# Optimization experiments

Hardware: AMD Instinct MI355X
Metric: run time of the kernel (lower is better)

## Reference

```python
import jax, jax.numpy as jnp
import numpy as np

N = 8192      # nodes
E = 262144    # edges (avg degree 32)
IN_DIM = 512
H1 = 256
H2 = 128


def _graph_conv(x, src, dst, W, b, act):
    """DGL GraphConv with norm='both', allow_zero_in_degree=True.
    h = D_in^{-1/2} * A @ (D_out^{-1/2} * x @ W) + b, then activation.
    Degrees clamped to min 1 (DGL behavior)."""
    ones = jnp.ones((src.shape[0],), dtype=x.dtype)
    deg_out = jax.ops.segment_sum(ones, src, num_segments=N)
    deg_in = jax.ops.segment_sum(ones, dst, num_segments=N)
    norm_src = jnp.maximum(deg_out, 1.0) ** -0.5  # [N]
    norm_dst = jnp.maximum(deg_in, 1.0) ** -0.5   # [N]
    # apply weight before aggregation (out_feats < in_feats, as DGL does)
    h = (x * norm_src[:, None]) @ W               # [N, out]
    agg = jax.ops.segment_sum(h[src], dst, num_segments=N)  # gather-scatter SpMM
    return act(agg * norm_dst[:, None] + b)


def setup_inputs() -> dict:
    key = jax.random.key(0)
    ks = jax.random.split(key, 7)
    features = jax.random.normal(ks[0], (N, IN_DIM), dtype=jnp.float32)
    src = jax.random.randint(ks[1], (E,), 0, N)
    dst = jax.random.randint(ks[2], (E,), 0, N)
    W1 = jax.random.normal(ks[3], (IN_DIM, H1), dtype=jnp.float32) * (1.0 / np.sqrt(IN_DIM))
    b1 = jnp.zeros((H1,), dtype=jnp.float32)
    W2 = jax.random.normal(ks[4], (H1, H2), dtype=jnp.float32) * (1.0 / np.sqrt(H1))
    b2 = jnp.zeros((H2,), dtype=jnp.float32)
    return {"features": features, "src": src, "dst": dst,
            "W1": W1, "b1": b1, "W2": W2, "b2": b2}


def reference(features, src, dst, W1, b1, W2, b2):
    x = _graph_conv(features, src, dst, W1, b1, jax.nn.relu)
    emb = _graph_conv(x, src, dst, W2, b2, lambda a: a)
    logits = jax.nn.sigmoid(emb @ emb.T)  # [N, N] dense reconstruction
    return (emb, logits)
```

## Files before the change

kernel.cpp:

```cpp
#include <hip/hip_runtime.h>

#define NN 8192
#define EE 262144
#define IN_DIM 512
#define HD1 256
#define HD2 128

typedef __attribute__((ext_vector_type(8))) short bf16x8;
typedef __attribute__((ext_vector_type(4))) float f32x4;

__device__ inline unsigned short f2bf(float f) {
    unsigned int u = __builtin_bit_cast(unsigned int, f);
    u += 0x7fffu + ((u >> 16) & 1u);
    return (unsigned short)(u >> 16);
}


__global__ void deg_kernel(const int* __restrict__ src, const int* __restrict__ dst,
                           int* __restrict__ deg_out, int* __restrict__ deg_in) {
    int e = blockIdx.x * blockDim.x + threadIdx.x;
    if (e < EE) {
        atomicAdd(&deg_out[src[e]], 1);
        atomicAdd(&deg_in[dst[e]], 1);
    }
}

__global__ void norm_kernel(const int* __restrict__ deg_out, const int* __restrict__ deg_in,
                            float* __restrict__ norm_src, float* __restrict__ norm_dst) {
    int i = blockIdx.x * blockDim.x + threadIdx.x;
    if (i < NN) {
        int dout = deg_out[i]; if (dout < 1) dout = 1;
        int din  = deg_in[i];  if (din  < 1) din  = 1;
        norm_src[i] = rsqrtf((float)dout);
        norm_dst[i] = rsqrtf((float)din);
    }
}

__global__ void scan_kernel(const int* __restrict__ counts, int* __restrict__ row_start) {
    __shared__ int sums[256];
    int t = threadIdx.x;
    int base = t * 32;
    int local[32];
    int s = 0;
    for (int i = 0; i < 32; i++) { local[i] = s; s += counts[base + i]; }
    sums[t] = s;
    __syncthreads();
    for (int off = 1; off < 256; off <<= 1) {
        int v = (t >= off) ? sums[t - off] : 0;
        __syncthreads();
        sums[t] += v;
        __syncthreads();
    }
    int coff = (t == 0) ? 0 : sums[t - 1];
    for (int i = 0; i < 32; i++) row_start[base + i] = coff + local[i];
    if (t == 255) row_start[NN] = sums[255];
}

__global__ void fill_kernel(const int* __restrict__ src, const int* __restrict__ dst,
                            const int* __restrict__ row_start, int* __restrict__ cursor,
                            int* __restrict__ eidx) {
    int e = blockIdx.x * blockDim.x + threadIdx.x;
    if (e < EE) {
        int d = dst[e];
        int pos = atomicAdd(&cursor[d], 1);
        eidx[row_start[d] + pos] = src[e];
    }
}


__global__ void scale_cast_kernel(const float4* __restrict__ x, const float* __restrict__ norm_src,
                                  ushort4* __restrict__ out) {
    int idx = blockIdx.x * blockDim.x + threadIdx.x;
    if (idx < NN * IN_DIM / 4) {
        float ns = norm_src[idx >> 7];
        float4 v = x[idx];
        ushort4 o;
        o.x = f2bf(v.x * ns); o.y = f2bf(v.y * ns);
        o.z = f2bf(v.z * ns); o.w = f2bf(v.w * ns);
        out[idx] = o;
    }
}

__global__ void transpose_cast_kernel(const float* __restrict__ W, unsigned short* __restrict__ Wt,
                                      int K, int Nc) {
    int idx = blockIdx.x * blockDim.x + threadIdx.x;
    if (idx < K * Nc) {
        int n = idx / K;
        int k = idx - n * K;
        Wt[idx] = f2bf(W[k * Nc + n]);
    }
}

template <int EPI>
__global__ __launch_bounds__(256) void gemm_tn(const short* __restrict__ A,
                                               const short* __restrict__ B,
                                               float* __restrict__ C, int N, int K) {
    int wave = threadIdx.x >> 6;
    int lane = threadIdx.x & 63;
    int wr = wave >> 1, wc = wave & 1;
    int row0 = blockIdx.y * 128 + wr * 64;
    int col0 = blockIdx.x * 128 + wc * 64;
    int l15 = lane & 15, q = lane >> 4;

    f32x4 acc[4][4] = {};
    const short* Abase = A + (size_t)(row0 + l15) * K + q * 8;
    const short* Bbase = B + (size_t)(col0 + l15) * K + q * 8;
    int nk = K >> 5;
    for (int ks = 0; ks < nk; ks++) {
        bf16x8 a[4], b[4];
#pragma unroll
        for (int t = 0; t < 4; t++) {
            a[t] = *(const bf16x8*)(Abase + (size_t)t * 16 * K + ks * 32);
            b[t] = *(const bf16x8*)(Bbase + (size_t)t * 16 * K + ks * 32);
        }
#pragma unroll
        for (int ti = 0; ti < 4; ti++)
#pragma unroll
            for (int tj = 0; tj < 4; tj++)
                acc[ti][tj] = __builtin_amdgcn_mfma_f32_16x16x32_bf16(a[ti], b[tj], acc[ti][tj], 0, 0, 0);
    }
#pragma unroll
    for (int ti = 0; ti < 4; ti++) {
#pragma unroll
        for (int tj = 0; tj < 4; tj++) {
#pragma unroll
            for (int r = 0; r < 4; r++) {
                int row = row0 + ti * 16 + q * 4 + r;
                int col = col0 + tj * 16 + l15;
                float v = acc[ti][tj][r];
                if (EPI == 1) v = __builtin_amdgcn_rcpf(1.0f + __expf(-v));
                C[(size_t)row * N + col] = v;
            }
        }
    }
}


__global__ void spmm1_kernel(const float* __restrict__ h1, const int* __restrict__ row_start,
                             const int* __restrict__ eidx, const float* __restrict__ norm_dst,
                             const float* __restrict__ norm_src, const float* __restrict__ b1,
                             unsigned short* __restrict__ x1n) {
    int r = blockIdx.x;
    int t = threadIdx.x;
    int s = row_start[r], e = row_start[r + 1];
    float sum = 0.0f;
    int i = s;
    for (; i + 4 <= e; i += 4) {
        int n0 = eidx[i], n1 = eidx[i + 1], n2 = eidx[i + 2], n3 = eidx[i + 3];
        float v0 = h1[n0 * HD1 + t];
        float v1 = h1[n1 * HD1 + t];
        float v2 = h1[n2 * HD1 + t];
        float v3 = h1[n3 * HD1 + t];
        sum += v0 + v1 + v2 + v3;
    }
    for (; i < e; i++) sum += h1[eidx[i] * HD1 + t];
    float x = sum * norm_dst[r] + b1[t];
    x = fmaxf(x, 0.0f) * norm_src[r];
    x1n[r * HD1 + t] = f2bf(x);
}

__global__ void spmm2_kernel(const float* __restrict__ h2, const int* __restrict__ row_start,
                             const int* __restrict__ eidx, const float* __restrict__ norm_dst,
                             const float* __restrict__ b2, float* __restrict__ emb,
                             unsigned short* __restrict__ embb) {
    int r = blockIdx.x;
    int t = threadIdx.x;
    int s = row_start[r], e = row_start[r + 1];
    float sum = 0.0f;
    int i = s;
    for (; i + 4 <= e; i += 4) {
        int n0 = eidx[i], n1 = eidx[i + 1], n2 = eidx[i + 2], n3 = eidx[i + 3];
        float v0 = h2[n0 * HD2 + t];
        float v1 = h2[n1 * HD2 + t];
        float v2 = h2[n2 * HD2 + t];
        float v3 = h2[n3 * HD2 + t];
        sum += v0 + v1 + v2 + v3;
    }
    for (; i < e; i++) sum += h2[eidx[i] * HD2 + t];
    float x = sum * norm_dst[r] + b2[t];
    emb[r * HD2 + t] = x;
    embb[r * HD2 + t] = f2bf(x);
}


extern "C" void kernel_launch(void* const* d_in, const int* in_sizes, int n_in,
                              void* d_out, int out_size, void* d_ws, size_t ws_size,
                              hipStream_t stream) {
    const float* features = (const float*)d_in[0];
    const int* src = (const int*)d_in[1];
    const int* dst = (const int*)d_in[2];
    const float* W1 = (const float*)d_in[3];
    const float* b1 = (const float*)d_in[4];
    const float* W2 = (const float*)d_in[5];
    const float* b2 = (const float*)d_in[6];

    char* ws = (char*)d_ws;
    size_t o = 0;
    auto alloc = [&](size_t bytes) -> char* {
        char* p = ws + o;
        o = (o + bytes + 255) & ~(size_t)255;
        return p;
    };
    int* deg_out = (int*)alloc(NN * 4);
    int* deg_in  = (int*)alloc(NN * 4);
    int* cursor  = (int*)alloc(NN * 4);
    float* norm_src = (float*)alloc(NN * 4);
    float* norm_dst = (float*)alloc(NN * 4);
    int* row_start  = (int*)alloc((NN + 1) * 4);
    int* eidx       = (int*)alloc(EE * 4);
    unsigned short* xn  = (unsigned short*)alloc((size_t)NN * IN_DIM * 2);
    unsigned short* w1t = (unsigned short*)alloc((size_t)HD1 * IN_DIM * 2);
    unsigned short* w2t = (unsigned short*)alloc((size_t)HD2 * HD1 * 2);
    float* h1 = (float*)alloc((size_t)NN * HD1 * 4);
    unsigned short* x1n = (unsigned short*)alloc((size_t)NN * HD1 * 2);
    float* h2 = (float*)alloc((size_t)NN * HD2 * 4);
    unsigned short* embb = (unsigned short*)alloc((size_t)NN * HD2 * 2);

    float* emb_out = (float*)d_out;
    float* logits_out = emb_out + (size_t)NN * HD2;

    hipMemsetAsync(deg_out, 0, (size_t)NN * 4 * 3, stream);

    deg_kernel<<<EE / 256, 256, 0, stream>>>(src, dst, deg_out, deg_in);
    norm_kernel<<<NN / 256, 256, 0, stream>>>(deg_out, deg_in, norm_src, norm_dst);
    scan_kernel<<<1, 256, 0, stream>>>(deg_in, row_start);
    fill_kernel<<<EE / 256, 256, 0, stream>>>(src, dst, row_start, cursor, eidx);

    scale_cast_kernel<<<(NN * IN_DIM / 4) / 256, 256, 0, stream>>>(
        (const float4*)features, norm_src, (ushort4*)xn);
    transpose_cast_kernel<<<(IN_DIM * HD1 + 255) / 256, 256, 0, stream>>>(W1, w1t, IN_DIM, HD1);
    transpose_cast_kernel<<<(HD1 * HD2 + 255) / 256, 256, 0, stream>>>(W2, w2t, HD1, HD2);

    gemm_tn<0><<<dim3(HD1 / 128, NN / 128), 256, 0, stream>>>(
        (const short*)xn, (const short*)w1t, h1, HD1, IN_DIM);
    spmm1_kernel<<<NN, HD1, 0, stream>>>(h1, row_start, eidx, norm_dst, norm_src, b1, x1n);

    gemm_tn<0><<<dim3(HD2 / 128, NN / 128), 256, 0, stream>>>(
        (const short*)x1n, (const short*)w2t, h2, HD2, HD1);
    spmm2_kernel<<<NN, HD2, 0, stream>>>(h2, row_start, eidx, norm_dst, b2, emb_out, embb);

    gemm_tn<1><<<dim3(NN / 128, NN / 128), 256, 0, stream>>>(
        (const short*)embb, (const short*)embb, logits_out, NN, HD2);
}
```

Before: 433.3 us.

## Vectorize logits stores, use bf16 intermediates, and fuse preprocessing kernels

The logits GEMM epilogue now writes float4 rows by exploiting the symmetry of emb·embᵀ, so each lane stores a transposed contiguous 4-float chunk instead of scattered scalars. The h1 and h2 intermediates are stored as bf16, with the source-norm scaling folded into the first GEMM epilogue. The SpMM kernels switch to one wave per row with vectorized bf16 gathers. The norm and scan kernels are merged, and the casts are merged into one kernel. This reduces store transactions and gather bandwidth, at the cost of extra bf16 rounding of intermediates and reliance on output symmetry.

After: 448.4 us. 1.03x slower.

```diff
diff --git a/kernel.cpp b/kernel.cpp
--- a/kernel.cpp
+++ b/kernel.cpp
@@ -13,6 +13,9 @@
     unsigned int u = __builtin_bit_cast(unsigned int, f);
     u += 0x7fffu + ((u >> 16) & 1u);
     return (unsigned short)(u >> 16);
+}
+__device__ inline float bf2f(unsigned short u) {
+    return __builtin_bit_cast(float, ((unsigned int)u) << 16);
 }
 
 
@@ -25,24 +28,20 @@
     }
 }
 
-__global__ void norm_kernel(const int* __restrict__ deg_out, const int* __restrict__ deg_in,
-                            float* __restrict__ norm_src, float* __restrict__ norm_dst) {
-    int i = blockIdx.x * blockDim.x + threadIdx.x;
-    if (i < NN) {
-        int dout = deg_out[i]; if (dout < 1) dout = 1;
-        int din  = deg_in[i];  if (din  < 1) din  = 1;
-        norm_src[i] = rsqrtf((float)dout);
-        norm_dst[i] = rsqrtf((float)din);
-    }
-}
-
-__global__ void scan_kernel(const int* __restrict__ counts, int* __restrict__ row_start) {
+__global__ void scan_norm_kernel(const int* __restrict__ deg_in, const int* __restrict__ deg_out,
+                                 int* __restrict__ row_start,
+                                 float* __restrict__ norm_src, float* __restrict__ norm_dst) {
     __shared__ int sums[256];
     int t = threadIdx.x;
     int base = t * 32;
+    int4 c[8];
+#pragma unroll
+    for (int i = 0; i < 8; i++) c[i] = ((const int4*)deg_in)[t * 8 + i];
+    const int* ci = (const int*)c;
     int local[32];
     int s = 0;
-    for (int i = 0; i < 32; i++) { local[i] = s; s += counts[base + i]; }
+#pragma unroll
+    for (int i = 0; i < 32; i++) { local[i] = s; s += ci[i]; }
     sums[t] = s;
     __syncthreads();
     for (int off = 1; off < 256; off <<= 1) {
@@ -52,8 +51,16 @@
         __syncthreads();
     }
     int coff = (t == 0) ? 0 : sums[t - 1];
+#pragma unroll
     for (int i = 0; i < 32; i++) row_start[base + i] = coff + local[i];
     if (t == 255) row_start[NN] = sums[255];
+    for (int i = 0; i < 32; i++) {
+        int idx = i * 256 + t;
+        int dout = deg_out[idx]; if (dout < 1) dout = 1;
+        int din  = deg_in[idx];  if (din  < 1) din  = 1;
+        norm_src[idx] = rsqrtf((float)dout);
+        norm_dst[idx] = rsqrtf((float)din);
+    }
 }
 
 __global__ void fill_kernel(const int* __restrict__ src, const int* __restrict__ dst,
@@ -68,33 +75,38 @@
 }
 
 
-__global__ void scale_cast_kernel(const float4* __restrict__ x, const float* __restrict__ norm_src,
-                                  ushort4* __restrict__ out) {
-    int idx = blockIdx.x * blockDim.x + threadIdx.x;
-    if (idx < NN * IN_DIM / 4) {
-        float ns = norm_src[idx >> 7];
+#define XN_QUADS (NN * IN_DIM / 4)
+#define W1_ELEMS (IN_DIM * HD1)
+#define W2_ELEMS (HD1 * HD2)
+
+__global__ void cast_all_kernel(const float4* __restrict__ x, ushort4* __restrict__ xn,
+                                const float* __restrict__ W1, unsigned short* __restrict__ w1t,
+                                const float* __restrict__ W2, unsigned short* __restrict__ w2t) {
+    int idx = blockIdx.x * 256 + threadIdx.x;
+    if (idx < XN_QUADS) {
         float4 v = x[idx];
         ushort4 o;
-        o.x = f2bf(v.x * ns); o.y = f2bf(v.y * ns);
-        o.z = f2bf(v.z * ns); o.w = f2bf(v.w * ns);
-        out[idx] = o;
-    }
-}
-
-__global__ void transpose_cast_kernel(const float* __restrict__ W, unsigned short* __restrict__ Wt,
-                                      int K, int Nc) {
-    int idx = blockIdx.x * blockDim.x + threadIdx.x;
-    if (idx < K * Nc) {
-        int n = idx / K;
-        int k = idx - n * K;
-        Wt[idx] = f2bf(W[k * Nc + n]);
+        o.x = f2bf(v.x); o.y = f2bf(v.y); o.z = f2bf(v.z); o.w = f2bf(v.w);
+        xn[idx] = o;
+    } else if (idx < XN_QUADS + W1_ELEMS) {
+        int j = idx - XN_QUADS;
+        int n = j >> 9;
+        int k = j & (IN_DIM - 1);
+        w1t[j] = f2bf(W1[k * HD1 + n]);
+    } else if (idx < XN_QUADS + W1_ELEMS + W2_ELEMS) {
+        int j = idx - XN_QUADS - W1_ELEMS;
+        int n = j >> 8;
+        int k = j & (HD1 - 1);
+        w2t[j] = f2bf(W2[k * HD2 + n]);
     }
 }
 
 template <int EPI>
 __global__ __launch_bounds__(256) void gemm_tn(const short* __restrict__ A,
                                                const short* __restrict__ B,
-                                               float* __restrict__ C, int N, int K) {
+                                               void* __restrict__ Cv,
+                                               const float* __restrict__ rownorm,
+                                               int N, int K) {
     int wave = threadIdx.x >> 6;
     int lane = threadIdx.x & 63;
     int wr = wave >> 1, wc = wave & 1;
@@ -119,67 +131,105 @@
             for (int tj = 0; tj < 4; tj++)
                 acc[ti][tj] = __builtin_amdgcn_mfma_f32_16x16x32_bf16(a[ti], b[tj], acc[ti][tj], 0, 0, 0);
     }
-#pragma unroll
-    for (int ti = 0; ti < 4; ti++) {
-#pragma unroll
-        for (int tj = 0; tj < 4; tj++) {
-#pragma unroll
-            for (int r = 0; r < 4; r++) {
-                int row = row0 + ti * 16 + q * 4 + r;
-                int col = col0 + tj * 16 + l15;
-                float v = acc[ti][tj][r];
-                if (EPI == 1) v = __builtin_amdgcn_rcpf(1.0f + __expf(-v));
-                C[(size_t)row * N + col] = v;
+
+    if (EPI == 1) {
+        float* C = (float*)Cv;
+#pragma unroll
+        for (int ti = 0; ti < 4; ti++) {
+#pragma unroll
+            for (int tj = 0; tj < 4; tj++) {
+                int row = col0 + tj * 16 + l15;
+                int colb = row0 + ti * 16 + q * 4;
+                float4 v;
+                float* vp = (float*)&v;
+#pragma unroll
+                for (int r = 0; r < 4; r++) {
+                    float x = acc[ti][tj][r];
+                    vp[r] = __builtin_amdgcn_rcpf(1.0f + __expf(-x));
+                }
+                *(float4*)(C + (size_t)row * N + colb) = v;
             }
         }
-    }
-}
-
-
-__global__ void spmm1_kernel(const float* __restrict__ h1, const int* __restrict__ row_start,
+    } else {
+        unsigned short* C = (unsigned short*)Cv;
+#pragma unroll
+        for (int ti = 0; ti < 4; ti++) {
+#pragma unroll
+            for (int tj = 0; tj < 4; tj++) {
+#pragma unroll
+                for (int r = 0; r < 4; r++) {
+                    int row = row0 + ti * 16 + q * 4 + r;
+                    int col = col0 + tj * 16 + l15;
+                    float v = acc[ti][tj][r];
+                    if (EPI == 2) v *= rownorm[row];
+                    C[(size_t)row * N + col] = f2bf(v);
+                }
+            }
+        }
+    }
+}
+
+
+__global__ void spmm1_kernel(const ushort4* __restrict__ h1b, const int* __restrict__ row_start,
                              const int* __restrict__ eidx, const float* __restrict__ norm_dst,
-                             const float* __restrict__ norm_src, const float* __restrict__ b1,
-                             unsigned short* __restrict__ x1n) {
-    int r = blockIdx.x;
-    int t = threadIdx.x;
+                             const float* __restrict__ norm_src, const float4* __restrict__ b1,
+                             ushort4* __restrict__ x1n) {
+    int lane = threadIdx.x & 63;
+    int r = blockIdx.x * 4 + (threadIdx.x >> 6);
     int s = row_start[r], e = row_start[r + 1];
-    float sum = 0.0f;
+    float sx = 0.f, sy = 0.f, sz = 0.f, sw = 0.f;
     int i = s;
-    for (; i + 4 <= e; i += 4) {
-        int n0 = eidx[i], n1 = eidx[i + 1], n2 = eidx[i + 2], n3 = eidx[i + 3];
-        float v0 = h1[n0 * HD1 + t];
-        float v1 = h1[n1 * HD1 + t];
-        float v2 = h1[n2 * HD1 + t];
-        float v3 = h1[n3 * HD1 + t];
-        sum += v0 + v1 + v2 + v3;
-    }
-    for (; i < e; i++) sum += h1[eidx[i] * HD1 + t];
-    float x = sum * norm_dst[r] + b1[t];
-    x = fmaxf(x, 0.0f) * norm_src[r];
-    x1n[r * HD1 + t] = f2bf(x);
-}
-
-__global__ void spmm2_kernel(const float* __restrict__ h2, const int* __restrict__ row_start,
+    for (; i + 2 <= e; i += 2) {
+        int n0 = eidx[i], n1 = eidx[i + 1];
+        ushort4 v0 = h1b[n0 * 64 + lane];
+        ushort4 v1 = h1b[n1 * 64 + lane];
+        sx += bf2f(v0.x) + bf2f(v1.x);
+        sy += bf2f(v0.y) + bf2f(v1.y);
+        sz += bf2f(v0.z) + bf2f(v1.z);
+        sw += bf2f(v0.w) + bf2f(v1.w);
+    }
+    if (i < e) {
+        ushort4 v0 = h1b[eidx[i] * 64 + lane];
+        sx += bf2f(v0.x); sy += bf2f(v0.y); sz += bf2f(v0.z); sw += bf2f(v0.w);
+    }
+    float nd = norm_dst[r], ns = norm_src[r];
+    float4 bb = b1[lane];
+    ushort4 o;
+    o.x = f2bf(fmaxf(sx * nd + bb.x, 0.f) * ns);
+    o.y = f2bf(fmaxf(sy * nd + bb.y, 0.f) * ns);
+    o.z = f2bf(fmaxf(sz * nd + bb.z, 0.f) * ns);
+    o.w = f2bf(fmaxf(sw * nd + bb.w, 0.f) * ns);
+    x1n[r * 64 + lane] = o;
+}
+
+__global__ void spmm2_kernel(const ushort2* __restrict__ h2b, const int* __restrict__ row_start,
                              const int* __restrict__ eidx, const float* __restrict__ norm_dst,
-                             const float* __restrict__ b2, float* __restrict__ emb,
-                             unsigned short* __restrict__ embb) {
-    int r = blockIdx.x;
-    int t = threadIdx.x;
+                             const float2* __restrict__ b2, float2* __restrict__ emb,
+                             ushort2* __restrict__ embb) {
+    int lane = threadIdx.x & 63;
+    int r = blockIdx.x * 4 + (threadIdx.x >> 6);
     int s = row_start[r], e = row_start[r + 1];
-    float sum = 0.0f;
+    float sx = 0.f, sy = 0.f;
     int i = s;
-    for (; i + 4 <= e; i += 4) {
-        int n0 = eidx[i], n1 = eidx[i + 1], n2 = eidx[i + 2], n3 = eidx[i + 3];
-        float v0 = h2[n0 * HD2 + t];
-        float v1 = h2[n1 * HD2 + t];
-        float v2 = h2[n2 * HD2 + t];
-        float v3 = h2[n3 * HD2 + t];
-        sum += v0 + v1 + v2 + v3;
-    }
-    for (; i < e; i++) sum += h2[eidx[i] * HD2 + t];
-    float x = sum * norm_dst[r] + b2[t];
-    emb[r * HD2 + t] = x;
-    embb[r * HD2 + t] = f2bf(x);
+    for (; i + 2 <= e; i += 2) {
+        int n0 = eidx[i], n1 = eidx[i + 1];
+        ushort2 v0 = h2b[n0 * 64 + lane];
+        ushort2 v1 = h2b[n1 * 64 + lane];
+        sx += bf2f(v0.x) + bf2f(v1.x);
+        sy += bf2f(v0.y) + bf2f(v1.y);
+    }
+    if (i < e) {
+        ushort2 v0 = h2b[eidx[i] * 64 + lane];
+        sx += bf2f(v0.x); sy += bf2f(v0.y);
+    }
+    float nd = norm_dst[r];
+    float2 bb = b2[lane];
+    float x0 = sx * nd + bb.x;
+    float x1 = sy * nd + bb.y;
+    float2 eo; eo.x = x0; eo.y = x1;
+    emb[r * 64 + lane] = eo;
+    ushort2 bo; bo.x = f2bf(x0); bo.y = f2bf(x1);
+    embb[r * 64 + lane] = bo;
 }
 
 
@@ -211,9 +261,9 @@
     unsigned short* xn  = (unsigned short*)alloc((size_t)NN * IN_DIM * 2);
     unsigned short* w1t = (unsigned short*)alloc((size_t)HD1 * IN_DIM * 2);
     unsigned short* w2t = (unsigned short*)alloc((size_t)HD2 * HD1 * 2);
-    float* h1 = (float*)alloc((size_t)NN * HD1 * 4);
+    unsigned short* h1b = (unsigned short*)alloc((size_t)NN * HD1 * 2);
     unsigned short* x1n = (unsigned short*)alloc((size_t)NN * HD1 * 2);
-    float* h2 = (float*)alloc((size_t)NN * HD2 * 4);
+    unsigned short* h2b = (unsigned short*)alloc((size_t)NN * HD2 * 2);
     unsigned short* embb = (unsigned short*)alloc((size_t)NN * HD2 * 2);
 
     float* emb_out = (float*)d_out;
@@ -221,24 +271,24 @@
 
     hipMemsetAsync(deg_out, 0, (size_t)NN * 4 * 3, stream);
 
+    cast_all_kernel<<<(XN_QUADS + W1_ELEMS + W2_ELEMS) / 256, 256, 0, stream>>>(
+        (const float4*)features, (ushort4*)xn, W1, w1t, W2, w2t);
     deg_kernel<<<EE / 256, 256, 0, stream>>>(src, dst, deg_out, deg_in);
-    norm_kernel<<<NN / 256, 256, 0, stream>>>(deg_out, deg_in, norm_src, norm_dst);
-    scan_kernel<<<1, 256, 0, stream>>>(deg_in, row_start);
+    scan_norm_kernel<<<1, 256, 0, stream>>>(deg_in, deg_out, row_start, norm_src, norm_dst);
     fill_kernel<<<EE / 256, 256, 0, stream>>>(src, dst, row_start, cursor, eidx);
 
-    scale_cast_kernel<<<(NN * IN_DIM / 4) / 256, 256, 0, stream>>>(
-        (const float4*)features, norm_src, (ushort4*)xn);
-    transpose_cast_kernel<<<(IN_DIM * HD1 + 255) / 256, 256, 0, stream>>>(W1, w1t, IN_DIM, HD1);
-    transpose_cast_kernel<<<(HD1 * HD2 + 255) / 256, 256, 0, stream>>>(W2, w2t, HD1, HD2);
-
-    gemm_tn<0><<<dim3(HD1 / 128, NN / 128), 256, 0, stream>>>(
-        (const short*)xn, (const short*)w1t, h1, HD1, IN_DIM);
-    spmm1_kernel<<<NN, HD1, 0, stream>>>(h1, row_start, eidx, norm_dst, norm_src, b1, x1n);
-
-    gemm_tn<0><<<dim3(HD2 / 128, NN / 128), 256, 0, stream>>>(
-        (const short*)x1n, (const short*)w2t, h2, HD2, HD1);
-    spmm2_kernel<<<NN, HD2, 0, stream>>>(h2, row_start, eidx, norm_dst, b2, emb_out, embb);
+    gemm_tn<2><<<dim3(HD1 / 128, NN / 128), 256, 0, stream>>>(
+        (const short*)xn, (const short*)w1t, h1b, norm_src, HD1, IN_DIM);
+    spmm1_kernel<<<NN / 4, 256, 0, stream>>>((const ushort4*)h1b, row_start, eidx,
+                                             norm_dst, norm_src, (const float4*)b1,
+                                             (ushort4*)x1n);
+
+    gemm_tn<3><<<dim3(HD2 / 128, NN / 128), 256, 0, stream>>>(
+        (const short*)x1n, (const short*)w2t, h2b, nullptr, HD2, HD1);
+    spmm2_kernel<<<NN / 4, 256, 0, stream>>>((const ushort2*)h2b, row_start, eidx,
+                                             norm_dst, (const float2*)b2,
+                                             (float2*)emb_out, (ushort2*)embb);
 
     gemm_tn<1><<<dim3(NN / 128, NN / 128), 256, 0, stream>>>(
-        (const short*)embb, (const short*)embb, logits_out, NN, HD2);
-}
+        (const short*)embb, (const short*)embb, logits_out, nullptr, NN, HD2);
+}
```
